# Optimization experiments

Measured on AMD Instinct MI355X. Metric: run time of the kernel, lower is better.

The kernel has to match this reference:

```python
import jax, jax.numpy as jnp
import numpy as np

N, NFEAT, NHID, NCLASS = 384, 512, 192, 64


def setup_inputs() -> dict:
    key = jax.random.key(0)
    ks = jax.random.split(key, 16)
    s = 0.05
    inp = {
        "x": jax.random.normal(ks[0], (N, NFEAT), jnp.float32),
        # normalized dense adjacency surrogates (row-scaled so outputs stay O(1))
        "adj": jax.random.uniform(ks[1], (N, N), jnp.float32) / N,
        "adj1": jax.random.uniform(ks[2], (N, N * N), jnp.float32) / (N * N),
        # nn.Linear emb / cls
        "W_emb": jax.random.normal(ks[3], (NFEAT, NHID), jnp.float32) * s,
        "b_emb": jnp.zeros((NHID,), jnp.float32),
        "W_cls": jax.random.normal(ks[4], (NHID, NCLASS), jnp.float32) * s,
        "b_cls": jnp.zeros((NCLASS,), jnp.float32),
        # GraphConvolution gc1, gc2
        "W1": jax.random.normal(ks[5], (NHID, NHID), jnp.float32) * s,
        "b1": jnp.zeros((NHID,), jnp.float32),
        "W2": jax.random.normal(ks[6], (NHID, NHID), jnp.float32) * s,
        "b2": jnp.zeros((NHID,), jnp.float32),
        # GraphConvolution_edge gc_e, gc_e2
        "We": jax.random.normal(ks[7], (NHID, NHID), jnp.float32) * s,
        "be": jnp.zeros((NHID,), jnp.float32),
        "We2": jax.random.normal(ks[8], (NHID, NHID), jnp.float32) * s,
        "be2": jnp.zeros((NHID,), jnp.float32),
    }
    return inp


def _outer_edge(a, b):
    # [N,H] x [N,H] -> [N*N, H] elementwise outer-product edge features
    n, h = a.shape
    return (a[:, None, :] * b[None, :, :]).reshape(n * n, h)


def reference(x, adj, adj1, W_emb, b_emb, W_cls, b_cls, W1, b1, W2, b2, We, be, We2, be2):
    # eval mode: dropout is identity
    x_init = x @ W_emb + b_emb                      # [N,H]
    edge_feat = _outer_edge(x_init, x_init)          # [N*N,H]
    # gc_e: adj1 @ (edge_feat @ We) + be
    x_e = jax.nn.relu(adj1 @ (edge_feat @ We) + be)  # [N,H]
    # gc1: adj @ (x_init @ W1) + b1
    x1 = jax.nn.relu(adj @ (x_init @ W1) + b1)       # [N,H]
    xs = x1 + x_e + x_init
    x_mid = adj @ (xs @ W2) + b2                     # gc2
    edge_feat1 = _outer_edge(x1, x1)                 # [N*N,H]
    x_e2 = adj1 @ ((edge_feat + edge_feat1) @ We2) + be2  # gc_e2
    h = jax.nn.relu(x_mid + x_e2)
    logits = h @ W_cls + b_cls                       # [N,C]
    return jax.nn.log_softmax(logits, axis=1)
```

## Files before the change

kernel.cpp:

```cpp
#include <hip/hip_runtime.h>

#define NN 384
#define NF 512
#define NH 192
#define NC 64

typedef __bf16 bf16x8 __attribute__((ext_vector_type(8)));
typedef float f32x4 __attribute__((ext_vector_type(4)));

static __device__ __forceinline__ float b2f(unsigned short u) {
  union { unsigned int i; float f; } v; v.i = ((unsigned int)u) << 16; return v.f;
}
static __device__ __forceinline__ unsigned short f2b(float f) {
  unsigned int u = __float_as_uint(f);
  unsigned int r = (u + 0x7FFFu + ((u >> 16) & 1u)) >> 16;
  return (unsigned short)r;
}

__global__ void __launch_bounds__(192) k_emb(
    const float* __restrict__ x, const float* __restrict__ W_emb,
    const float* __restrict__ b_emb, const float* __restrict__ W1,
    float* __restrict__ xinit, float* __restrict__ t1,
    unsigned short* __restrict__ uT)
{
  __shared__ float xl[2][NF];
  __shared__ float xi[2][NH];
  const int r0 = blockIdx.x * 2;
  const int tid = threadIdx.x;
#pragma unroll
  for (int rr = 0; rr < 2; ++rr)
    for (int k = tid; k < NF; k += 192)
      xl[rr][k] = x[(size_t)(r0 + rr) * NF + k];
  __syncthreads();
  const int h = tid;
  float a0 = b_emb[h], a1 = a0;
  for (int k = 0; k < NF; ++k) {
    float w = W_emb[k * NH + h];
    a0 += xl[0][k] * w; a1 += xl[1][k] * w;
  }
  float acc[2] = {a0, a1};
#pragma unroll
  for (int rr = 0; rr < 2; ++rr) {
    xinit[(r0 + rr) * NH + h] = acc[rr];
    xi[rr][h] = acc[rr];
    uT[h * NN + (r0 + rr)] = f2b(acc[rr]);
  }
  __syncthreads();
  float c0 = 0.f, c1 = 0.f;
  for (int k = 0; k < NH; ++k) {
    float w = W1[k * NH + h];
    c0 += xi[0][k] * w; c1 += xi[1][k] * w;
  }
  t1[(r0 + 0) * NH + h] = c0;
  t1[(r0 + 1) * NH + h] = c1;
}

__global__ void __launch_bounds__(192) k_gc1(
    const float* __restrict__ adj, const float* __restrict__ t1,
    const float* __restrict__ b1, float* __restrict__ x1,
    unsigned short* __restrict__ vT)
{
  __shared__ float al[2][NN];
  const int r0 = blockIdx.x * 2;
  const int tid = threadIdx.x;
#pragma unroll
  for (int rr = 0; rr < 2; ++rr)
    for (int j = tid; j < NN; j += 192)
      al[rr][j] = adj[(size_t)(r0 + rr) * NN + j];
  __syncthreads();
  const int h = tid;
  float a0 = b1[h], a1 = a0;
  for (int j = 0; j < NN; ++j) {
    float t = t1[j * NH + h];
    a0 += al[0][j] * t; a1 += al[1][j] * t;
  }
  float acc[2] = {a0, a1};
#pragma unroll
  for (int rr = 0; rr < 2; ++rr) {
    float v = fmaxf(acc[rr], 0.f);
    x1[(r0 + rr) * NH + h] = v;
    vT[h * NN + (r0 + rr)] = f2b(v);
  }
}

__global__ void __launch_bounds__(512, 2) k_edge(
    const float* __restrict__ adj1, const unsigned short* __restrict__ uT,
    const unsigned short* __restrict__ vT,
    float* __restrict__ E0p, float* __restrict__ E1p)
{
  __shared__ __align__(16) unsigned char lds_raw[163840];

  const int tid = threadIdx.x;
  const int wv = tid >> 6, l = tid & 63;
  const int lr = l & 15, lg = l >> 4;
  const int rg = wv >> 2, hg = (wv >> 1) & 1, uv = wv & 1;
  const int bid = blockIdx.x;
  const int r = bid / 3, ig = bid - r * 3;
  const int i0 = ig * 128;
  const float* __restrict__ Ar = adj1 + (size_t)r * (NN * NN);
  const unsigned short* __restrict__ selT = uv ? vT : uT;

  const int aunit = (l & 7) ^ (l >> 3);
  const int bunit = (l & 3) ^ ((l >> 3) & 3);

  f32x4 acc[4][6];
  const f32x4 zero = {0.f, 0.f, 0.f, 0.f};
#pragma unroll
  for (int s = 0; s < 4; ++s)
#pragma unroll
    for (int t = 0; t < 6; ++t) acc[s][t] = zero;

  auto STAGE = [&](int slot, int kb) {
    float* As = (float*)(lds_raw + slot * 40960);
    unsigned short* Bs = (unsigned short*)(lds_raw + slot * 40960 + 16384);
#pragma unroll
    for (int p = 0; p < 2; ++p) {
      const int rowbase = wv * 16 + p * 8;
      const float* g = Ar + (size_t)(i0 + rowbase + (l >> 3)) * NN + kb + 4 * aunit;
      __builtin_amdgcn_global_load_lds(
          (const __attribute__((address_space(1))) unsigned int*)g,
          (__attribute__((address_space(3))) unsigned int*)(As + rowbase * 32),
          16, 0, 0);
    }
#pragma unroll
    for (int q = 0; q < 3; ++q) {
      const int m = wv * 3 + q;
      const int uvs = (m >= 12) ? 1 : 0;
      const int H0 = (m - uvs * 12) * 16;
      const unsigned short* src =
          (uvs ? vT : uT) + (H0 + (l >> 2)) * NN + kb + 8 * bunit;
      __builtin_amdgcn_global_load_lds(
          (const __attribute__((address_space(1))) unsigned int*)src,
          (__attribute__((address_space(3))) unsigned int*)(Bs + uvs * 6144 + H0 * 32),
          16, 0, 0);
    }
  };

  STAGE(0, 0);
  STAGE(1, 32);
  STAGE(2, 64);

#pragma unroll
  for (int kk = 0; kk < 12; ++kk) {
    if (kk <= 9)       asm volatile("s_waitcnt vmcnt(10)" ::: "memory");
    else if (kk == 10) asm volatile("s_waitcnt vmcnt(5)" ::: "memory");
    else               asm volatile("s_waitcnt vmcnt(0)" ::: "memory");
    __builtin_amdgcn_sched_barrier(0);
    __builtin_amdgcn_s_barrier();

    const int slot = kk & 3;
    const float* Ab = (const float*)(lds_raw + slot * 40960);
    const unsigned short* Bb =
        (const unsigned short*)(lds_raw + slot * 40960 + 16384) + uv * 6144;

    bf16x8 bfr[6];
#pragma unroll
    for (int t = 0; t < 6; ++t) {
      const int h = (hg * 6 + t) * 16 + lr;
      bfr[t] = *reinterpret_cast<const bf16x8*>(Bb + h * 32 + 8 * (lg ^ ((lr >> 1) & 3)));
    }
#pragma unroll
    for (int s = 0; s < 4; ++s) {
      const int R = rg * 64 + s * 16 + lr;
      const float* rowp = Ab + R * 32;
      f32x4 q0 = *reinterpret_cast<const f32x4*>(rowp + 4 * ((2 * lg) ^ (lr & 7)));
      f32x4 q1 = *reinterpret_cast<const f32x4*>(rowp + 4 * (((2 * lg) + 1) ^ (lr & 7)));
      bf16x8 af;
      af[0] = (__bf16)q0[0]; af[1] = (__bf16)q0[1];
      af[2] = (__bf16)q0[2]; af[3] = (__bf16)q0[3];
      af[4] = (__bf16)q1[0]; af[5] = (__bf16)q1[1];
      af[6] = (__bf16)q1[2]; af[7] = (__bf16)q1[3];
#pragma unroll
      for (int t = 0; t < 6; ++t)
        acc[s][t] = __builtin_amdgcn_mfma_f32_16x16x32_bf16(af, bfr[t], acc[s][t], 0, 0, 0);
    }

    if (kk <= 8) STAGE((kk + 3) & 3, (kk + 3) * 32);
  }

  float e[6];
#pragma unroll
  for (int t = 0; t < 6; ++t) {
    const int h = (hg * 6 + t) * 16 + lr;
    float ac = 0.f;
#pragma unroll
    for (int s = 0; s < 4; ++s) {
      const int ii = i0 + rg * 64 + s * 16 + lg * 4;
      ushort4 w4 = *reinterpret_cast<const ushort4*>(selT + h * NN + ii);
      ac += b2f(w4.x) * acc[s][t][0] + b2f(w4.y) * acc[s][t][1]
          + b2f(w4.z) * acc[s][t][2] + b2f(w4.w) * acc[s][t][3];
    }
    ac += __shfl_xor(ac, 16);
    ac += __shfl_xor(ac, 32);
    e[t] = ac;
  }
  __syncthreads();
  float* scratch = (float*)lds_raw;
  if (rg == 1 && lg == 0) {
#pragma unroll
    for (int t = 0; t < 6; ++t)
      scratch[uv * 192 + (hg * 6 + t) * 16 + lr] = e[t];
  }
  __syncthreads();
  if (rg == 0 && lg == 0) {
    float* Ep = uv ? E1p : E0p;
#pragma unroll
    for (int t = 0; t < 6; ++t) {
      const int h = (hg * 6 + t) * 16 + lr;
      Ep[((size_t)ig * NN + r) * NH + h] = e[t] + scratch[uv * 192 + h];
    }
  }
}

__global__ void __launch_bounds__(192) k_mid(
    const float* __restrict__ E0p, const float* __restrict__ E1p,
    const float* __restrict__ x1, const float* __restrict__ xinit,
    const float* __restrict__ We, const float* __restrict__ be,
    const float* __restrict__ W2, const float* __restrict__ We2,
    const float* __restrict__ be2, float* __restrict__ t2,
    float* __restrict__ xe2)
{
  __shared__ float e0l[2][NH], s01[2][NH], xsl[2][NH];
  const int r0 = blockIdx.x * 2;
  const int h = threadIdx.x;
#pragma unroll
  for (int rr = 0; rr < 2; ++rr) {
    const int idx = (r0 + rr) * NH + h;
    float e0v = E0p[idx] + E0p[NN * NH + idx] + E0p[2 * NN * NH + idx];
    float e1v = E1p[idx] + E1p[NN * NH + idx] + E1p[2 * NN * NH + idx];
    e0l[rr][h] = e0v;
    s01[rr][h] = e0v + e1v;
  }
  __syncthreads();
  float x0 = be[h], x1a = x0;
  for (int k = 0; k < NH; ++k) {
    float w = We[k * NH + h];
    x0 += e0l[0][k] * w; x1a += e0l[1][k] * w;
  }
  float xe[2] = {x0, x1a};
#pragma unroll
  for (int rr = 0; rr < 2; ++rr) {
    const int idx = (r0 + rr) * NH + h;
    xsl[rr][h] = fmaxf(xe[rr], 0.f) + x1[idx] + xinit[idx];
  }
  __syncthreads();
  float t0 = 0.f, t1v = 0.f;
  float b0 = be2[h], b1v = b0;
  for (int k = 0; k < NH; ++k) {
    float w2 = W2[k * NH + h];
    float w3 = We2[k * NH + h];
    t0 += xsl[0][k] * w2; t1v += xsl[1][k] * w2;
    b0 += s01[0][k] * w3; b1v += s01[1][k] * w3;
  }
  t2[(r0 + 0) * NH + h] = t0;  t2[(r0 + 1) * NH + h] = t1v;
  xe2[(r0 + 0) * NH + h] = b0; xe2[(r0 + 1) * NH + h] = b1v;
}

__global__ void __launch_bounds__(256) k_out(
    const float* __restrict__ adj, const float* __restrict__ t2,
    const float* __restrict__ b2, const float* __restrict__ xe2,
    const float* __restrict__ Wc, const float* __restrict__ bc,
    float* __restrict__ out)
{
  __shared__ float al[2][NN];
  __shared__ float hl[2][NH];
  const int r0 = blockIdx.x * 2;
  const int tid = threadIdx.x;
#pragma unroll
  for (int rr = 0; rr < 2; ++rr)
    for (int j = tid; j < NN; j += 256)
      al[rr][j] = adj[(size_t)(r0 + rr) * NN + j];
  __syncthreads();
  if (tid < NH) {
    const int h = tid;
    float a0 = b2[h], a1 = a0;
    for (int j = 0; j < NN; ++j) {
      float t = t2[j * NH + h];
      a0 += al[0][j] * t; a1 += al[1][j] * t;
    }
    float acc[2] = {a0, a1};
#pragma unroll
    for (int rr = 0; rr < 2; ++rr)
      hl[rr][h] = fmaxf(acc[rr] + xe2[(r0 + rr) * NH + h], 0.f);
  }
  __syncthreads();
  const int w = tid >> 6, lane = tid & 63;
  if (w < 2) {
    float lgt = bc[lane];
    for (int k = 0; k < NH; ++k) lgt += hl[w][k] * Wc[k * NC + lane];
    float m = lgt;
#pragma unroll
    for (int off = 32; off >= 1; off >>= 1) m = fmaxf(m, __shfl_xor(m, off));
    float s = expf(lgt - m);
#pragma unroll
    for (int off = 32; off >= 1; off >>= 1) s += __shfl_xor(s, off);
    out[(size_t)(r0 + w) * NC + lane] = lgt - m - logf(s);
  }
}

extern "C" void kernel_launch(void* const* d_in, const int* in_sizes, int n_in,
                              void* d_out, int out_size, void* d_ws, size_t ws_size,
                              hipStream_t stream) {
  const float* x     = (const float*)d_in[0];
  const float* adj   = (const float*)d_in[1];
  const float* adj1  = (const float*)d_in[2];
  const float* W_emb = (const float*)d_in[3];
  const float* b_emb = (const float*)d_in[4];
  const float* W_cls = (const float*)d_in[5];
  const float* b_cls = (const float*)d_in[6];
  const float* W1    = (const float*)d_in[7];
  const float* b1    = (const float*)d_in[8];
  const float* W2    = (const float*)d_in[9];
  const float* b2    = (const float*)d_in[10];
  const float* We    = (const float*)d_in[11];
  const float* be    = (const float*)d_in[12];
  const float* We2   = (const float*)d_in[13];
  const float* be2   = (const float*)d_in[14];

  char* ws = (char*)d_ws;
  float* xinit = (float*)(ws + 0);
  float* t1    = (float*)(ws + 294912);
  float* x1    = (float*)(ws + 589824);
  float* E0p   = (float*)(ws + 884736);
  float* E1p   = (float*)(ws + 1769472);
  unsigned short* uT = (unsigned short*)(ws + 2654208);
  unsigned short* vT = (unsigned short*)(ws + 2801664);
  float* t2  = E0p;
  float* xe2 = E0p + NN * NH;

  k_emb<<<192, 192, 0, stream>>>(x, W_emb, b_emb, W1, xinit, t1, uT);
  k_gc1<<<192, 192, 0, stream>>>(adj, t1, b1, x1, vT);
  k_edge<<<1152, 512, 0, stream>>>(adj1, uT, vT, E0p, E1p);
  k_mid<<<192, 192, 0, stream>>>(E0p, E1p, x1, xinit, We, be, W2, We2, be2, t2, xe2);
  k_out<<<192, 256, 0, stream>>>(adj, t2, b2, xe2, W_cls, b_cls, (float*)d_out);
}
```

Before: 163.2 us.

## Double edge-kernel waves and split A/B staging with smaller LDS buffers

```diff
diff --git a/kernel.cpp b/kernel.cpp
--- a/kernel.cpp
+++ b/kernel.cpp
@@ -83,12 +83,12 @@
   }
 }
 
-__global__ void __launch_bounds__(512, 2) k_edge(
+__global__ void __launch_bounds__(1024, 4) k_edge(
     const float* __restrict__ adj1, const unsigned short* __restrict__ uT,
     const unsigned short* __restrict__ vT,
     float* __restrict__ E0p, float* __restrict__ E1p)
 {
-  __shared__ __align__(16) unsigned char lds_raw[163840];
+  __shared__ __align__(16) unsigned char lds_raw[114688];
 
   const int tid = threadIdx.x;
   const int wv = tid >> 6, l = tid & 63;
@@ -100,58 +100,56 @@
   const float* __restrict__ Ar = adj1 + (size_t)r * (NN * NN);
   const unsigned short* __restrict__ selT = uv ? vT : uT;
 
-  const int aunit = (l & 7) ^ (l >> 3);
-  const int bunit = (l & 3) ^ ((l >> 3) & 3);
-
-  f32x4 acc[4][6];
-  const f32x4 zero = {0.f, 0.f, 0.f, 0.f};
-#pragma unroll
-  for (int s = 0; s < 4; ++s)
-#pragma unroll
-    for (int t = 0; t < 6; ++t) acc[s][t] = zero;
-
-  auto STAGE = [&](int slot, int kb) {
-    float* As = (float*)(lds_raw + slot * 40960);
-    unsigned short* Bs = (unsigned short*)(lds_raw + slot * 40960 + 16384);
-#pragma unroll
-    for (int p = 0; p < 2; ++p) {
-      const int rowbase = wv * 16 + p * 8;
-      const float* g = Ar + (size_t)(i0 + rowbase + (l >> 3)) * NN + kb + 4 * aunit;
-      __builtin_amdgcn_global_load_lds(
-          (const __attribute__((address_space(1))) unsigned int*)g,
-          (__attribute__((address_space(3))) unsigned int*)(As + rowbase * 32),
-          16, 0, 0);
-    }
-#pragma unroll
-    for (int q = 0; q < 3; ++q) {
-      const int m = wv * 3 + q;
-      const int uvs = (m >= 12) ? 1 : 0;
+  const int arow = tid >> 3;
+  const int aunit = (tid & 7) ^ (arow & 7);
+  auto STAGE_A = [&](int slot, int kb) {
+    const float* g = Ar + (size_t)(i0 + arow) * NN + kb + 4 * aunit;
+    __builtin_amdgcn_global_load_lds(
+        (const __attribute__((address_space(1))) unsigned int*)g,
+        (__attribute__((address_space(3))) unsigned int*)(lds_raw + slot * 16384 + wv * 1024),
+        16, 0, 0);
+  };
+  auto STAGE_B = [&](int slot, int kb) {
+#pragma unroll
+    for (int q = 0; q < 2; ++q) {
+      int m = wv * 2 + q;
+      if (m >= 24) m -= 24;
+      const int uvs = m / 12;
       const int H0 = (m - uvs * 12) * 16;
       const unsigned short* src =
-          (uvs ? vT : uT) + (H0 + (l >> 2)) * NN + kb + 8 * bunit;
+          (uvs ? vT : uT) + (H0 + (l >> 2)) * NN + kb + 8 * ((l & 3) ^ ((l >> 3) & 3));
       __builtin_amdgcn_global_load_lds(
           (const __attribute__((address_space(1))) unsigned int*)src,
-          (__attribute__((address_space(3))) unsigned int*)(Bs + uvs * 6144 + H0 * 32),
+          (__attribute__((address_space(3))) unsigned int*)
+              (lds_raw + 65536 + slot * 24576 + (uvs * 6144 + H0 * 32) * 2),
           16, 0, 0);
     }
   };
 
-  STAGE(0, 0);
-  STAGE(1, 32);
-  STAGE(2, 64);
+  f32x4 acc[2][6];
+  const f32x4 zero = {0.f, 0.f, 0.f, 0.f};
+#pragma unroll
+  for (int s = 0; s < 2; ++s)
+#pragma unroll
+    for (int t = 0; t < 6; ++t) acc[s][t] = zero;
+
+  STAGE_A(0, 0);
+  STAGE_B(0, 0);
+  STAGE_A(1, 32);
+  STAGE_A(2, 64);
 
 #pragma unroll
   for (int kk = 0; kk < 12; ++kk) {
-    if (kk <= 9)       asm volatile("s_waitcnt vmcnt(10)" ::: "memory");
-    else if (kk == 10) asm volatile("s_waitcnt vmcnt(5)" ::: "memory");
-    else               asm volatile("s_waitcnt vmcnt(0)" ::: "memory");
+    if (kk == 0)      asm volatile("s_waitcnt vmcnt(2)" ::: "memory");
+    else if (kk <= 9) asm volatile("s_waitcnt vmcnt(1)" ::: "memory");
+    else              asm volatile("s_waitcnt vmcnt(0)" ::: "memory");
     __builtin_amdgcn_sched_barrier(0);
     __builtin_amdgcn_s_barrier();
-
-    const int slot = kk & 3;
-    const float* Ab = (const float*)(lds_raw + slot * 40960);
+    __builtin_amdgcn_sched_barrier(0);
+
+    const float* Ab = (const float*)(lds_raw + (kk & 3) * 16384);
     const unsigned short* Bb =
-        (const unsigned short*)(lds_raw + slot * 40960 + 16384) + uv * 6144;
+        (const unsigned short*)(lds_raw + 65536 + (kk & 1) * 24576) + uv * 6144;
 
     bf16x8 bfr[6];
 #pragma unroll
@@ -160,11 +158,11 @@
       bfr[t] = *reinterpret_cast<const bf16x8*>(Bb + h * 32 + 8 * (lg ^ ((lr >> 1) & 3)));
     }
 #pragma unroll
-    for (int s = 0; s < 4; ++s) {
-      const int R = rg * 64 + s * 16 + lr;
+    for (int s = 0; s < 2; ++s) {
+      const int R = rg * 32 + s * 16 + lr;
       const float* rowp = Ab + R * 32;
-      f32x4 q0 = *reinterpret_cast<const f32x4*>(rowp + 4 * ((2 * lg) ^ (lr & 7)));
-      f32x4 q1 = *reinterpret_cast<const f32x4*>(rowp + 4 * (((2 * lg) + 1) ^ (lr & 7)));
+      f32x4 q0 = *reinterpret_cast<const f32x4*>(rowp + 4 * ((2 * lg) ^ (R & 7)));
+      f32x4 q1 = *reinterpret_cast<const f32x4*>(rowp + 4 * ((2 * lg + 1) ^ (R & 7)));
       bf16x8 af;
       af[0] = (__bf16)q0[0]; af[1] = (__bf16)q0[1];
       af[2] = (__bf16)q0[2]; af[3] = (__bf16)q0[3];
@@ -175,7 +173,8 @@
         acc[s][t] = __builtin_amdgcn_mfma_f32_16x16x32_bf16(af, bfr[t], acc[s][t], 0, 0, 0);
     }
 
-    if (kk <= 8) STAGE((kk + 3) & 3, (kk + 3) * 32);
+    if (kk < 11) STAGE_B((kk + 1) & 1, (kk + 1) * 32);
+    if (kk <= 8) STAGE_A((kk + 3) & 3, (kk + 3) * 32);
   }
 
   float e[6];
@@ -184,8 +183,8 @@
     const int h = (hg * 6 + t) * 16 + lr;
     float ac = 0.f;
 #pragma unroll
-    for (int s = 0; s < 4; ++s) {
-      const int ii = i0 + rg * 64 + s * 16 + lg * 4;
+    for (int s = 0; s < 2; ++s) {
+      const int ii = i0 + rg * 32 + s * 16 + lg * 4;
       ushort4 w4 = *reinterpret_cast<const ushort4*>(selT + h * NN + ii);
       ac += b2f(w4.x) * acc[s][t][0] + b2f(w4.y) * acc[s][t][1]
           + b2f(w4.z) * acc[s][t][2] + b2f(w4.w) * acc[s][t][3];
@@ -196,18 +195,20 @@
   }
   __syncthreads();
   float* scratch = (float*)lds_raw;
-  if (rg == 1 && lg == 0) {
+  if (lg == 0) {
 #pragma unroll
     for (int t = 0; t < 6; ++t)
-      scratch[uv * 192 + (hg * 6 + t) * 16 + lr] = e[t];
+      scratch[((uv * 2 + hg) * 4 + rg) * 96 + t * 16 + lr] = e[t];
   }
   __syncthreads();
   if (rg == 0 && lg == 0) {
     float* Ep = uv ? E1p : E0p;
+    const float* base = scratch + (uv * 2 + hg) * 4 * 96;
 #pragma unroll
     for (int t = 0; t < 6; ++t) {
       const int h = (hg * 6 + t) * 16 + lr;
-      Ep[((size_t)ig * NN + r) * NH + h] = e[t] + scratch[uv * 192 + h];
+      const int o = t * 16 + lr;
+      Ep[((size_t)ig * NN + r) * NH + h] = base[o] + base[96 + o] + base[192 + o] + base[288 + o];
     }
   }
 }
@@ -330,7 +331,7 @@
 
   k_emb<<<192, 192, 0, stream>>>(x, W_emb, b_emb, W1, xinit, t1, uT);
   k_gc1<<<192, 192, 0, stream>>>(adj, t1, b1, x1, vT);
-  k_edge<<<1152, 512, 0, stream>>>(adj1, uT, vT, E0p, E1p);
+  k_edge<<<1152, 1024, 0, stream>>>(adj1, uT, vT, E0p, E1p);
   k_mid<<<192, 192, 0, stream>>>(E0p, E1p, x1, xinit, We, be, W2, We2, be2, t2, xe2);
   k_out<<<192, 256, 0, stream>>>(adj, t2, b2, xe2, W_cls, b_cls, (float*)d_out);
 }
```

Measured after the change: 182.1 us. +11.5%, slower.

## Replace LDS-staged edge GEMM with direct global-to-register loads and swapped MFMA operands

Applied to the files above, without the earlier changes.

```diff
diff --git a/kernel.cpp b/kernel.cpp
--- a/kernel.cpp
+++ b/kernel.cpp
@@ -83,132 +83,127 @@
   }
 }
 
-__global__ void __launch_bounds__(512, 2) k_edge(
+__global__ void __launch_bounds__(512, 1) k_edge(
     const float* __restrict__ adj1, const unsigned short* __restrict__ uT,
     const unsigned short* __restrict__ vT,
     float* __restrict__ E0p, float* __restrict__ E1p)
 {
-  __shared__ __align__(16) unsigned char lds_raw[163840];
+  __shared__ float red[2][2][2][96];
 
   const int tid = threadIdx.x;
   const int wv = tid >> 6, l = tid & 63;
   const int lr = l & 15, lg = l >> 4;
   const int rg = wv >> 2, hg = (wv >> 1) & 1, uv = wv & 1;
-  const int bid = blockIdx.x;
-  const int r = bid / 3, ig = bid - r * 3;
-  const int i0 = ig * 128;
+  const int r = blockIdx.x / 3, ig = blockIdx.x - r * 3;
   const float* __restrict__ Ar = adj1 + (size_t)r * (NN * NN);
   const unsigned short* __restrict__ selT = uv ? vT : uT;
 
-  const int aunit = (l & 7) ^ (l >> 3);
-  const int bunit = (l & 3) ^ ((l >> 3) & 3);
-
-  f32x4 acc[4][6];
-  const f32x4 zero = {0.f, 0.f, 0.f, 0.f};
-#pragma unroll
-  for (int s = 0; s < 4; ++s)
-#pragma unroll
-    for (int t = 0; t < 6; ++t) acc[s][t] = zero;
-
-  auto STAGE = [&](int slot, int kb) {
-    float* As = (float*)(lds_raw + slot * 40960);
-    unsigned short* Bs = (unsigned short*)(lds_raw + slot * 40960 + 16384);
-#pragma unroll
-    for (int p = 0; p < 2; ++p) {
-      const int rowbase = wv * 16 + p * 8;
-      const float* g = Ar + (size_t)(i0 + rowbase + (l >> 3)) * NN + kb + 4 * aunit;
-      __builtin_amdgcn_global_load_lds(
-          (const __attribute__((address_space(1))) unsigned int*)g,
-          (__attribute__((address_space(3))) unsigned int*)(As + rowbase * 32),
-          16, 0, 0);
-    }
-#pragma unroll
-    for (int q = 0; q < 3; ++q) {
-      const int m = wv * 3 + q;
-      const int uvs = (m >= 12) ? 1 : 0;
-      const int H0 = (m - uvs * 12) * 16;
-      const unsigned short* src =
-          (uvs ? vT : uT) + (H0 + (l >> 2)) * NN + kb + 8 * bunit;
-      __builtin_amdgcn_global_load_lds(
-          (const __attribute__((address_space(1))) unsigned int*)src,
-          (__attribute__((address_space(3))) unsigned int*)(Bs + uvs * 6144 + H0 * 32),
-          16, 0, 0);
-    }
-  };
-
-  STAGE(0, 0);
-  STAGE(1, 32);
-  STAGE(2, 64);
-
-#pragma unroll
-  for (int kk = 0; kk < 12; ++kk) {
-    if (kk <= 9)       asm volatile("s_waitcnt vmcnt(10)" ::: "memory");
-    else if (kk == 10) asm volatile("s_waitcnt vmcnt(5)" ::: "memory");
-    else               asm volatile("s_waitcnt vmcnt(0)" ::: "memory");
-    __builtin_amdgcn_sched_barrier(0);
-    __builtin_amdgcn_s_barrier();
-
-    const int slot = kk & 3;
-    const float* Ab = (const float*)(lds_raw + slot * 40960);
-    const unsigned short* Bb =
-        (const unsigned short*)(lds_raw + slot * 40960 + 16384) + uv * 6144;
-
-    bf16x8 bfr[6];
+  const unsigned short* ufp[6];
+#pragma unroll
+  for (int t = 0; t < 6; ++t)
+    ufp[t] = selT + ((hg * 6 + t) * 16 + lr) * NN + lg * 8;
+
+  float e[6][4];
+#pragma unroll
+  for (int t = 0; t < 6; ++t)
+#pragma unroll
+    for (int q = 0; q < 4; ++q) e[t][q] = 0.f;
+
+#pragma unroll
+  for (int p = 0; p < 2; ++p) {
+    const int i0p = ig * 128 + rg * 64 + p * 32;
+    const float* arow0 = Ar + (size_t)(i0p + lr) * NN + lg * 8;
+    const float* arow1 = Ar + (size_t)(i0p + 16 + lr) * NN + lg * 8;
+
+    f32x4 A[3][2][2];
+    bf16x8 uf[2][6];
+    f32x4 acc[2][6];
+    const f32x4 zero = {0.f, 0.f, 0.f, 0.f};
+#pragma unroll
+    for (int s = 0; s < 2; ++s)
+#pragma unroll
+      for (int t = 0; t < 6; ++t) acc[s][t] = zero;
+
+#pragma unroll
+    for (int s = 0; s < 2; ++s) {
+      const float* ar = s ? arow1 : arow0;
+      A[0][s][0] = *reinterpret_cast<const f32x4*>(ar);
+      A[0][s][1] = *reinterpret_cast<const f32x4*>(ar + 4);
+      A[1][s][0] = *reinterpret_cast<const f32x4*>(ar + 32);
+      A[1][s][1] = *reinterpret_cast<const f32x4*>(ar + 36);
+    }
+#pragma unroll
+    for (int t = 0; t < 6; ++t)
+      uf[0][t] = *reinterpret_cast<const bf16x8*>(ufp[t]);
+
+#pragma unroll
+    for (int n = 0; n < 12; ++n) {
+      if (n < 10) {
+        const int kb2 = (n + 2) * 32;
+#pragma unroll
+        for (int s = 0; s < 2; ++s) {
+          const float* ar = (s ? arow1 : arow0) + kb2;
+          A[(n + 2) % 3][s][0] = *reinterpret_cast<const f32x4*>(ar);
+          A[(n + 2) % 3][s][1] = *reinterpret_cast<const f32x4*>(ar + 4);
+        }
+      }
+      if (n < 11) {
+        const int kb1 = (n + 1) * 32;
+#pragma unroll
+        for (int t = 0; t < 6; ++t)
+          uf[(n + 1) & 1][t] = *reinterpret_cast<const bf16x8*>(ufp[t] + kb1);
+      }
+      bf16x8 af[2];
+#pragma unroll
+      for (int s = 0; s < 2; ++s) {
+        f32x4 q0 = A[n % 3][s][0], q1 = A[n % 3][s][1];
+        af[s][0] = (__bf16)q0[0]; af[s][1] = (__bf16)q0[1];
+        af[s][2] = (__bf16)q0[2]; af[s][3] = (__bf16)q0[3];
+        af[s][4] = (__bf16)q1[0]; af[s][5] = (__bf16)q1[1];
+        af[s][6] = (__bf16)q1[2]; af[s][7] = (__bf16)q1[3];
+      }
+#pragma unroll
+      for (int t = 0; t < 6; ++t) {
+        acc[0][t] = __builtin_amdgcn_mfma_f32_16x16x32_bf16(uf[n & 1][t], af[0], acc[0][t], 0, 0, 0);
+        acc[1][t] = __builtin_amdgcn_mfma_f32_16x16x32_bf16(uf[n & 1][t], af[1], acc[1][t], 0, 0, 0);
+      }
+    }
+
 #pragma unroll
     for (int t = 0; t < 6; ++t) {
-      const int h = (hg * 6 + t) * 16 + lr;
-      bfr[t] = *reinterpret_cast<const bf16x8*>(Bb + h * 32 + 8 * (lg ^ ((lr >> 1) & 3)));
-    }
-#pragma unroll
-    for (int s = 0; s < 4; ++s) {
-      const int R = rg * 64 + s * 16 + lr;
-      const float* rowp = Ab + R * 32;
-      f32x4 q0 = *reinterpret_cast<const f32x4*>(rowp + 4 * ((2 * lg) ^ (lr & 7)));
-      f32x4 q1 = *reinterpret_cast<const f32x4*>(rowp + 4 * (((2 * lg) + 1) ^ (lr & 7)));
-      bf16x8 af;
-      af[0] = (__bf16)q0[0]; af[1] = (__bf16)q0[1];
-      af[2] = (__bf16)q0[2]; af[3] = (__bf16)q0[3];
-      af[4] = (__bf16)q1[0]; af[5] = (__bf16)q1[1];
-      af[6] = (__bf16)q1[2]; af[7] = (__bf16)q1[3];
-#pragma unroll
-      for (int t = 0; t < 6; ++t)
-        acc[s][t] = __builtin_amdgcn_mfma_f32_16x16x32_bf16(af, bfr[t], acc[s][t], 0, 0, 0);
-    }
-
-    if (kk <= 8) STAGE((kk + 3) & 3, (kk + 3) * 32);
-  }
-
-  float e[6];
-#pragma unroll
-  for (int t = 0; t < 6; ++t) {
-    const int h = (hg * 6 + t) * 16 + lr;
-    float ac = 0.f;
-#pragma unroll
-    for (int s = 0; s < 4; ++s) {
-      const int ii = i0 + rg * 64 + s * 16 + lg * 4;
-      ushort4 w4 = *reinterpret_cast<const ushort4*>(selT + h * NN + ii);
-      ac += b2f(w4.x) * acc[s][t][0] + b2f(w4.y) * acc[s][t][1]
-          + b2f(w4.z) * acc[s][t][2] + b2f(w4.w) * acc[s][t][3];
-    }
-    ac += __shfl_xor(ac, 16);
-    ac += __shfl_xor(ac, 32);
-    e[t] = ac;
-  }
-  __syncthreads();
-  float* scratch = (float*)lds_raw;
-  if (rg == 1 && lg == 0) {
+#pragma unroll
+      for (int q = 0; q < 4; ++q) {
+        const int h = (hg * 6 + t) * 16 + lg * 4 + q;
+        e[t][q] += b2f(selT[h * NN + i0p + lr]) * acc[0][t][q]
+                 + b2f(selT[h * NN + i0p + 16 + lr]) * acc[1][t][q];
+      }
+    }
+  }
+
+#pragma unroll
+  for (int t = 0; t < 6; ++t)
+#pragma unroll
+    for (int q = 0; q < 4; ++q) {
+      float s = e[t][q];
+      s += __shfl_xor(s, 1); s += __shfl_xor(s, 2);
+      s += __shfl_xor(s, 4); s += __shfl_xor(s, 8);
+      e[t][q] = s;
+    }
+  if (lr == 0) {
 #pragma unroll
     for (int t = 0; t < 6; ++t)
-      scratch[uv * 192 + (hg * 6 + t) * 16 + lr] = e[t];
-  }
-  __syncthreads();
-  if (rg == 0 && lg == 0) {
-    float* Ep = uv ? E1p : E0p;
-#pragma unroll
-    for (int t = 0; t < 6; ++t) {
-      const int h = (hg * 6 + t) * 16 + lr;
-      Ep[((size_t)ig * NN + r) * NH + h] = e[t] + scratch[uv * 192 + h];
-    }
+#pragma unroll
+      for (int q = 0; q < 4; ++q)
+        red[uv][hg][rg][t * 16 + lg * 4 + q] = e[t][q];
+  }
+  __syncthreads();
+  if (tid < 384) {
+    const int uvx = tid / 192, rem = tid - uvx * 192;
+    const int hgx = rem / 96, o = rem - hgx * 96;
+    const int h = hgx * 96 + o;
+    float val = red[uvx][hgx][0][o] + red[uvx][hgx][1][o];
+    float* Ep = uvx ? E1p : E0p;
+    Ep[((size_t)ig * NN + r) * NH + h] = val;
   }
 }
 
```

After: 302.0 us. +85.0%, slower.

## Switch edge kernel to double-buffered 64-wide K tiles with early prefetch

Applied to the files above, without the earlier changes.

```diff
diff --git a/kernel.cpp b/kernel.cpp
--- a/kernel.cpp
+++ b/kernel.cpp
@@ -100,9 +100,6 @@
   const float* __restrict__ Ar = adj1 + (size_t)r * (NN * NN);
   const unsigned short* __restrict__ selT = uv ? vT : uT;
 
-  const int aunit = (l & 7) ^ (l >> 3);
-  const int bunit = (l & 3) ^ ((l >> 3) & 3);
-
   f32x4 acc[4][6];
   const f32x4 zero = {0.f, 0.f, 0.f, 0.f};
 #pragma unroll
@@ -111,71 +108,80 @@
     for (int t = 0; t < 6; ++t) acc[s][t] = zero;
 
   auto STAGE = [&](int slot, int kb) {
-    float* As = (float*)(lds_raw + slot * 40960);
-    unsigned short* Bs = (unsigned short*)(lds_raw + slot * 40960 + 16384);
-#pragma unroll
-    for (int p = 0; p < 2; ++p) {
-      const int rowbase = wv * 16 + p * 8;
-      const float* g = Ar + (size_t)(i0 + rowbase + (l >> 3)) * NN + kb + 4 * aunit;
+    float* As = (float*)(lds_raw + slot * 81920);
+    unsigned short* Bs = (unsigned short*)(lds_raw + slot * 81920 + 32768);
+#pragma unroll
+    for (int p = 0; p < 4; ++p) {
+      const int row = p * 32 + wv * 4 + (l >> 4);
+      const int u = l & 15;
+      const float* g = Ar + (size_t)(i0 + row) * NN + kb + 4 * (u ^ (row & 15));
       __builtin_amdgcn_global_load_lds(
           (const __attribute__((address_space(1))) unsigned int*)g,
-          (__attribute__((address_space(3))) unsigned int*)(As + rowbase * 32),
+          (__attribute__((address_space(3))) unsigned int*)(As + (p * 512 + wv * 64) * 4),
           16, 0, 0);
     }
 #pragma unroll
-    for (int q = 0; q < 3; ++q) {
-      const int m = wv * 3 + q;
-      const int uvs = (m >= 12) ? 1 : 0;
-      const int H0 = (m - uvs * 12) * 16;
+    for (int q = 0; q < 6; ++q) {
+      const int j = wv * 6 + q;
+      const int group = j >> 1, part = j & 1;
+      const int uvs = (group >= 12) ? 1 : 0;
+      const int H0 = (group - uvs * 12) * 16;
+      const int row = H0 + part * 8 + (l >> 3);
       const unsigned short* src =
-          (uvs ? vT : uT) + (H0 + (l >> 2)) * NN + kb + 8 * bunit;
+          (uvs ? vT : uT) + row * NN + kb + 8 * ((l & 7) ^ (l >> 3));
       __builtin_amdgcn_global_load_lds(
           (const __attribute__((address_space(1))) unsigned int*)src,
-          (__attribute__((address_space(3))) unsigned int*)(Bs + uvs * 6144 + H0 * 32),
+          (__attribute__((address_space(3))) unsigned int*)
+              (Bs + uvs * 12288 + (H0 + part * 8) * 64),
           16, 0, 0);
     }
   };
 
   STAGE(0, 0);
-  STAGE(1, 32);
-  STAGE(2, 64);
-
-#pragma unroll
-  for (int kk = 0; kk < 12; ++kk) {
-    if (kk <= 9)       asm volatile("s_waitcnt vmcnt(10)" ::: "memory");
-    else if (kk == 10) asm volatile("s_waitcnt vmcnt(5)" ::: "memory");
-    else               asm volatile("s_waitcnt vmcnt(0)" ::: "memory");
+
+#pragma unroll
+  for (int kk = 0; kk < 6; ++kk) {
+    asm volatile("s_waitcnt vmcnt(0)" ::: "memory");
     __builtin_amdgcn_sched_barrier(0);
     __builtin_amdgcn_s_barrier();
 
-    const int slot = kk & 3;
-    const float* Ab = (const float*)(lds_raw + slot * 40960);
+    if (kk < 5) STAGE((kk + 1) & 1, (kk + 1) * 64);
+    __builtin_amdgcn_sched_barrier(0);
+
+    const int slot = kk & 1;
+    const float* Ab = (const float*)(lds_raw + slot * 81920);
     const unsigned short* Bb =
-        (const unsigned short*)(lds_raw + slot * 40960 + 16384) + uv * 6144;
-
-    bf16x8 bfr[6];
-#pragma unroll
-    for (int t = 0; t < 6; ++t) {
-      const int h = (hg * 6 + t) * 16 + lr;
-      bfr[t] = *reinterpret_cast<const bf16x8*>(Bb + h * 32 + 8 * (lg ^ ((lr >> 1) & 3)));
-    }
+        (const unsigned short*)(lds_raw + slot * 81920 + 32768) + uv * 12288;
+
+    bf16x8 bfr[2][6];
+#pragma unroll
+    for (int kh = 0; kh < 2; ++kh)
+#pragma unroll
+      for (int t = 0; t < 6; ++t) {
+        const int h = (hg * 6 + t) * 16 + lr;
+        bfr[kh][t] = *reinterpret_cast<const bf16x8*>(
+            Bb + h * 64 + 8 * ((kh * 4 + lg) ^ (lr & 7)));
+      }
 #pragma unroll
     for (int s = 0; s < 4; ++s) {
       const int R = rg * 64 + s * 16 + lr;
-      const float* rowp = Ab + R * 32;
-      f32x4 q0 = *reinterpret_cast<const f32x4*>(rowp + 4 * ((2 * lg) ^ (lr & 7)));
-      f32x4 q1 = *reinterpret_cast<const f32x4*>(rowp + 4 * (((2 * lg) + 1) ^ (lr & 7)));
-      bf16x8 af;
-      af[0] = (__bf16)q0[0]; af[1] = (__bf16)q0[1];
-      af[2] = (__bf16)q0[2]; af[3] = (__bf16)q0[3];
-      af[4] = (__bf16)q1[0]; af[5] = (__bf16)q1[1];
-      af[6] = (__bf16)q1[2]; af[7] = (__bf16)q1[3];
-#pragma unroll
-      for (int t = 0; t < 6; ++t)
-        acc[s][t] = __builtin_amdgcn_mfma_f32_16x16x32_bf16(af, bfr[t], acc[s][t], 0, 0, 0);
-    }
-
-    if (kk <= 8) STAGE((kk + 3) & 3, (kk + 3) * 32);
+      const float* rowp = Ab + R * 64;
+#pragma unroll
+      for (int kh = 0; kh < 2; ++kh) {
+        f32x4 q0 = *reinterpret_cast<const f32x4*>(
+            rowp + 4 * ((kh * 8 + 2 * lg) ^ (R & 15)));
+        f32x4 q1 = *reinterpret_cast<const f32x4*>(
+            rowp + 4 * ((kh * 8 + 2 * lg + 1) ^ (R & 15)));
+        bf16x8 af;
+        af[0] = (__bf16)q0[0]; af[1] = (__bf16)q0[1];
+        af[2] = (__bf16)q0[2]; af[3] = (__bf16)q0[3];
+        af[4] = (__bf16)q1[0]; af[5] = (__bf16)q1[1];
+        af[6] = (__bf16)q1[2]; af[7] = (__bf16)q1[3];
+#pragma unroll
+        for (int t = 0; t < 6; ++t)
+          acc[s][t] = __builtin_amdgcn_mfma_f32_16x16x32_bf16(af, bfr[kh][t], acc[s][t], 0, 0, 0);
+      }
+    }
   }
 
   float e[6];
```

New measurement: 161.1 us. About the same (-1.3%).
